# Optimization experiments

Hardware: AMD Instinct MI355X
Metric: run time of the kernel (lower is better)

## Reference

```python
import jax, jax.numpy as jnp
import numpy as np

N = 4096
D = 256
L = 4
B = 8


def _graph_norm(x, cums, gamma, beta_g, num_segments):
    # GraphNormGAT: per-graph mean / unbiased std over ragged segments.
    n = x.shape[0]
    seg = jnp.searchsorted(cums, jnp.arange(n), side='right') - 1  # [N] segment ids
    ones = jnp.ones((n,), x.dtype)
    cnt = jax.ops.segment_sum(ones, seg, num_segments=num_segments)[:, None]  # [B,1]
    mean = jax.ops.segment_sum(x, seg, num_segments=num_segments) / cnt       # [B,D]
    diff = x - mean[seg]
    var = jax.ops.segment_sum(diff * diff, seg, num_segments=num_segments) / jnp.maximum(cnt - 1.0, 1.0)
    std = jnp.sqrt(var)
    return gamma * (diff / (std[seg] + 1e-5)) + beta_g


def _mean_shift(beta, xyz, q, k, v, y_hat, mask, t, bw, use_std_att, self_distance, max_iter):
    # Distance-masked mean-shift attention: Gaussian kernel on coordinates
    # combined with QK attention; iteratively shifts xyz toward weighted mean.
    d = q.shape[-1]
    x_out = v
    for _ in range(max_iter):
        att = (q @ k.T) * (1.0 / (np.sqrt(d) * float(t)))  # [N,N]
        if use_std_att:
            m = att.mean(axis=-1, keepdims=True)
            s = att.std(axis=-1, keepdims=True)
            att = (att - m) / (s + 1e-5)
        sq = jnp.sum(xyz * xyz, axis=-1)
        d2 = jnp.maximum(sq[:, None] + sq[None, :] - 2.0 * (xyz @ xyz.T), 0.0)
        d2 = d2 + float(self_distance) * jnp.eye(xyz.shape[0], dtype=d2.dtype)
        logits = att - d2 / (2.0 * bw * bw) + jnp.log(y_hat.T + 1e-9)
        logits = jnp.where(mask, logits, -1e9)
        w = jax.nn.softmax(logits, axis=-1)  # [N,N]
        xyz = beta * (w @ xyz) + (1.0 - beta) * xyz
        x_out = w @ v
    return xyz, x_out


def setup_inputs() -> dict:
    key = jax.random.key(0)
    ks = jax.random.split(key, 12)
    inp = {}
    inp['xyz'] = jax.random.normal(ks[0], (N, 3), jnp.float32)
    inp['x'] = jax.random.normal(ks[1], (N, D), jnp.float32)
    inp['y_hat'] = jax.random.uniform(ks[2], (N, 1), jnp.float32)
    inp['distance_mask'] = jax.random.randint(ks[3], (N, N), 0, 2).astype(bool)
    inp['t'] = 1
    inp['band_width'] = jnp.ones((1,), jnp.float32)
    inp['beta'] = jax.random.uniform(ks[4], (1,), jnp.float32)
    inp['cums'] = jnp.arange(B + 1, dtype=jnp.int32) * (N // B)
    inp['big_inter_mask'] = jnp.ones((N, N), dtype=bool)
    inp['use_std_att'] = 1
    inp['self_distance'] = 10000
    scale = 1.0 / np.sqrt(D)
    inp['qw'] = jax.random.normal(ks[5], (L, D, D), jnp.float32) * scale
    inp['kw'] = jax.random.normal(ks[6], (L, D, D), jnp.float32) * scale
    inp['vw'] = jax.random.normal(ks[7], (L, D, D), jnp.float32) * scale
    inp['ow'] = jax.random.normal(ks[8], (L, D, D), jnp.float32) * scale
    inp['qb'] = jnp.zeros((L, D), jnp.float32)
    inp['kb'] = jnp.zeros((L, D), jnp.float32)
    inp['vb'] = jnp.zeros((L, D), jnp.float32)
    inp['ob'] = jnp.zeros((L, D), jnp.float32)
    inp['gamma'] = jnp.ones((L, 1, D), jnp.float32)
    inp['beta_g'] = jnp.zeros((L, 1, D), jnp.float32)
    return inp


def reference(xyz, x, y_hat, distance_mask, t, band_width, beta, cums,
              big_inter_mask, use_std_att, self_distance,
              qw, kw, vw, ow, qb, kb, vb, ob, gamma, beta_g):
    mask = distance_mask & big_inter_mask
    bw = band_width[0]
    bt = beta[0]
    for l in range(L):
        res = x
        q = x @ qw[l].T + qb[l]
        k = x @ kw[l].T + kb[l]
        v = x @ vw[l].T + vb[l]
        xyz, h = _mean_shift(bt, xyz, q, k, v, y_hat, mask, t, bw,
                             use_std_att, self_distance, max_iter=1)
        h = h @ ow[l].T + ob[l]
        x = res + h
        x = _graph_norm(x, cums, gamma[l], beta_g[l], num_segments=B)
    return x
```

## Files before the change

### kernel.cpp

```cpp
#include <hip/hip_runtime.h>
#include <hip/hip_bf16.h>
#include <math.h>

#define N_ROWS 4096
#define DIM    256
#define LDQ    288
#define NLAYER 4
#define GN_CHUNKS 16

typedef __attribute__((ext_vector_type(8))) short bf16x8;
typedef __attribute__((ext_vector_type(4))) float f32x4;
typedef unsigned short us;

__device__ __forceinline__ us f2b(float f) {
  unsigned int u = __float_as_uint(f);
  unsigned int r = (u + 0x7fffu + ((u >> 16) & 1u)) >> 16;
  return (us)r;
}
__device__ __forceinline__ float b2f(us b) {
  return __uint_as_float(((unsigned int)b) << 16);
}
__device__ __forceinline__ bf16x8 f8_to_b8(float4 a, float4 b) {
  bf16x8 r;
  r[0] = (short)f2b(a.x);
  r[1] = (short)f2b(a.y);
  r[2] = (short)f2b(a.z);
  r[3] = (short)f2b(a.w);
  r[4] = (short)f2b(b.x);
  r[5] = (short)f2b(b.y);
  r[6] = (short)f2b(b.z);
  r[7] = (short)f2b(b.w);
  return r;
}
__device__ __forceinline__ void gload16(const us* g, short* l) {
  __builtin_amdgcn_global_load_lds(
      (const __attribute__((address_space(1))) unsigned int*)g,
      (__attribute__((address_space(3))) unsigned int*)l, 16, 0, 0);
}

__global__ __launch_bounds__(256) void mfma_nt_kernel(
    const us* __restrict__ A, int lda, const us* __restrict__ Bb,
    const float* __restrict__ Bf, const float* __restrict__ bias,
    const float* __restrict__ res, float* __restrict__ C) {
  __shared__ __align__(16) short Al[64 * 32];
  __shared__ __align__(16) short Bl[64 * 32];
  const int tid = threadIdx.x;
  const int wv = tid >> 6, lane = tid & 63;
  const int cl = lane & 15, gq = lane >> 4;
  const int wr = wv >> 1, wc = wv & 1;
  const int m0 = blockIdx.x * 64, n0 = blockIdx.y * 64;
  f32x4 acc[2][2];
#pragma unroll
  for (int mi = 0; mi < 2; ++mi)
#pragma unroll
    for (int ni = 0; ni < 2; ++ni) acc[mi][ni] = (f32x4){0.f, 0.f, 0.f, 0.f};
  for (int k0 = 0; k0 < DIM; k0 += 32) {
    __syncthreads();
    {
      int r = tid >> 2, c = tid & 3;
      *(bf16x8*)&Al[r * 32 + c * 8] =
          *(const bf16x8*)&A[(size_t)(m0 + r) * lda + k0 + c * 8];
      if (Bf) {
        float4 u = *(const float4*)&Bf[(size_t)(n0 + r) * DIM + k0 + c * 8];
        float4 v =
            *(const float4*)&Bf[(size_t)(n0 + r) * DIM + k0 + c * 8 + 4];
        *(bf16x8*)&Bl[r * 32 + c * 8] = f8_to_b8(u, v);
      } else {
        *(bf16x8*)&Bl[r * 32 + c * 8] =
            *(const bf16x8*)&Bb[(size_t)(n0 + r) * DIM + k0 + c * 8];
      }
    }
    __syncthreads();
    bf16x8 af[2], bfr[2];
#pragma unroll
    for (int mi = 0; mi < 2; ++mi)
      af[mi] = *(const bf16x8*)&Al[(wr * 32 + mi * 16 + cl) * 32 + gq * 8];
#pragma unroll
    for (int ni = 0; ni < 2; ++ni)
      bfr[ni] = *(const bf16x8*)&Bl[(wc * 32 + ni * 16 + cl) * 32 + gq * 8];
#pragma unroll
    for (int mi = 0; mi < 2; ++mi)
#pragma unroll
      for (int ni = 0; ni < 2; ++ni)
        acc[mi][ni] = __builtin_amdgcn_mfma_f32_16x16x32_bf16(
            af[mi], bfr[ni], acc[mi][ni], 0, 0, 0);
  }
#pragma unroll
  for (int mi = 0; mi < 2; ++mi)
#pragma unroll
    for (int ni = 0; ni < 2; ++ni)
#pragma unroll
      for (int i = 0; i < 4; ++i) {
        int row = m0 + wr * 32 + mi * 16 + gq * 4 + i;
        int col = n0 + wc * 32 + ni * 16 + cl;
        float v = acc[mi][ni][i];
        if (bias) v += bias[col];
        if (res) v += res[(size_t)row * DIM + col];
        C[(size_t)row * DIM + col] = v;
      }
}

__global__ __launch_bounds__(256) void mfma_qkv_kernel(
    const float* __restrict__ A, const float* __restrict__ W0,
    const float* __restrict__ W1, const float* __restrict__ W2,
    const float* __restrict__ b0, const float* __restrict__ b1,
    const float* __restrict__ b2, us* __restrict__ O0, us* __restrict__ O1,
    us* __restrict__ O2) {
  const float* Bm = (blockIdx.z == 0) ? W0 : (blockIdx.z == 1) ? W1 : W2;
  const float* bias = (blockIdx.z == 0) ? b0 : (blockIdx.z == 1) ? b1 : b2;
  us* Ob = (blockIdx.z == 0) ? O0 : (blockIdx.z == 1) ? O1 : O2;
  const int ldo = (blockIdx.z == 2) ? DIM : LDQ;
  __shared__ __align__(16) short Al[64 * 32];
  __shared__ __align__(16) short Bl[64 * 32];
  const int tid = threadIdx.x;
  const int wv = tid >> 6, lane = tid & 63;
  const int cl = lane & 15, gq = lane >> 4;
  const int wr = wv >> 1, wc = wv & 1;
  const int m0 = blockIdx.x * 64, n0 = blockIdx.y * 64;
  f32x4 acc[2][2];
#pragma unroll
  for (int mi = 0; mi < 2; ++mi)
#pragma unroll
    for (int ni = 0; ni < 2; ++ni) acc[mi][ni] = (f32x4){0.f, 0.f, 0.f, 0.f};
  for (int k0 = 0; k0 < DIM; k0 += 32) {
    __syncthreads();
    {
      int r = tid >> 2, c = tid & 3;
      float4 ua = *(const float4*)&A[(size_t)(m0 + r) * DIM + k0 + c * 8];
      float4 va = *(const float4*)&A[(size_t)(m0 + r) * DIM + k0 + c * 8 + 4];
      *(bf16x8*)&Al[r * 32 + c * 8] = f8_to_b8(ua, va);
      float4 ub = *(const float4*)&Bm[(size_t)(n0 + r) * DIM + k0 + c * 8];
      float4 vb = *(const float4*)&Bm[(size_t)(n0 + r) * DIM + k0 + c * 8 + 4];
      *(bf16x8*)&Bl[r * 32 + c * 8] = f8_to_b8(ub, vb);
    }
    __syncthreads();
    bf16x8 af[2], bfr[2];
#pragma unroll
    for (int mi = 0; mi < 2; ++mi)
      af[mi] = *(const bf16x8*)&Al[(wr * 32 + mi * 16 + cl) * 32 + gq * 8];
#pragma unroll
    for (int ni = 0; ni < 2; ++ni)
      bfr[ni] = *(const bf16x8*)&Bl[(wc * 32 + ni * 16 + cl) * 32 + gq * 8];
#pragma unroll
    for (int mi = 0; mi < 2; ++mi)
#pragma unroll
      for (int ni = 0; ni < 2; ++ni)
        acc[mi][ni] = __builtin_amdgcn_mfma_f32_16x16x32_bf16(
            af[mi], bfr[ni], acc[mi][ni], 0, 0, 0);
  }
#pragma unroll
  for (int mi = 0; mi < 2; ++mi)
#pragma unroll
    for (int ni = 0; ni < 2; ++ni)
#pragma unroll
      for (int i = 0; i < 4; ++i) {
        int row = m0 + wr * 32 + mi * 16 + gq * 4 + i;
        int col = n0 + wc * 32 + ni * 16 + cl;
        Ob[(size_t)row * ldo + col] = f2b(acc[mi][ni][i] + bias[col]);
      }
}

__global__ __launch_bounds__(256) void mpart_mfma_kernel(
    const us* __restrict__ Kt, float* __restrict__ Mp) {
  __shared__ __align__(16) short Al[64 * 32];
  __shared__ __align__(16) short Bl[64 * 32];
  const int tid = threadIdx.x;
  const int wv = tid >> 6, lane = tid & 63;
  const int cl = lane & 15, gq = lane >> 4;
  const int wr = wv >> 1, wc = wv & 1;
  const int a0 = blockIdx.x * 64, b0 = blockIdx.y * 64;
  const int kb = blockIdx.z * 512;
  f32x4 acc[2][2];
#pragma unroll
  for (int mi = 0; mi < 2; ++mi)
#pragma unroll
    for (int ni = 0; ni < 2; ++ni) acc[mi][ni] = (f32x4){0.f, 0.f, 0.f, 0.f};
  for (int k0 = 0; k0 < 512; k0 += 32) {
    __syncthreads();
    {
      int r = tid >> 2, c = tid & 3;
      *(bf16x8*)&Al[r * 32 + c * 8] =
          *(const bf16x8*)&Kt[(size_t)(a0 + r) * N_ROWS + kb + k0 + c * 8];
      *(bf16x8*)&Bl[r * 32 + c * 8] =
          *(const bf16x8*)&Kt[(size_t)(b0 + r) * N_ROWS + kb + k0 + c * 8];
    }
    __syncthreads();
    bf16x8 af[2], bfr[2];
#pragma unroll
    for (int mi = 0; mi < 2; ++mi)
      af[mi] = *(const bf16x8*)&Al[(wr * 32 + mi * 16 + cl) * 32 + gq * 8];
#pragma unroll
    for (int ni = 0; ni < 2; ++ni)
      bfr[ni] = *(const bf16x8*)&Bl[(wc * 32 + ni * 16 + cl) * 32 + gq * 8];
#pragma unroll
    for (int mi = 0; mi < 2; ++mi)
#pragma unroll
      for (int ni = 0; ni < 2; ++ni)
        acc[mi][ni] = __builtin_amdgcn_mfma_f32_16x16x32_bf16(
            af[mi], bfr[ni], acc[mi][ni], 0, 0, 0);
  }
#pragma unroll
  for (int mi = 0; mi < 2; ++mi)
#pragma unroll
    for (int ni = 0; ni < 2; ++ni)
#pragma unroll
      for (int i = 0; i < 4; ++i) {
        int row = a0 + wr * 32 + mi * 16 + gq * 4 + i;
        int col = b0 + wc * 32 + ni * 16 + cl;
        Mp[(size_t)blockIdx.z * 65536 + (size_t)row * DIM + col] =
            acc[mi][ni][i];
      }
}

__global__ void mreduce_kernel(const float* __restrict__ Mp,
                               us* __restrict__ Mb) {
  int e = blockIdx.x * 256 + threadIdx.x;
  float s = 0.f;
#pragma unroll
  for (int z = 0; z < 8; ++z) s += Mp[(size_t)z * 65536 + e];
  Mb[e] = f2b(s);
}

__global__ void ksum_part_kernel(const us* __restrict__ K,
                                 float* __restrict__ kpart) {
  int d = threadIdx.x, b = blockIdx.x;
  float s = 0.f;
  int base = b * 64;
  for (int n = 0; n < 64; ++n) s += b2f(K[(size_t)(base + n) * LDQ + d]);
  kpart[b * DIM + d] = s;
}
__global__ void ksum_red_kernel(const float* __restrict__ kpart,
                                float* __restrict__ ksum) {
  int d = threadIdx.x;
  float s = 0.f;
  for (int b = 0; b < 64; ++b) s += kpart[b * DIM + d];
  ksum[d] = s;
}

__global__ __launch_bounds__(256) void stats_kernel(
    us* __restrict__ Qh, us* __restrict__ Kh, us* __restrict__ Vtb,
    const float* __restrict__ tb, const float* __restrict__ ksum,
    const float* __restrict__ xyzc, const float* __restrict__ logy,
    const int* __restrict__ tptr, const float* __restrict__ bwp,
    const int* __restrict__ usestdp, float* __restrict__ c1a,
    float* __restrict__ cAa, float* __restrict__ colB) {
  const int wave = threadIdx.x >> 6, lane = threadIdx.x & 63;
  const int row = blockIdx.x * 4 + wave;
  ushort4 q4 = *(const ushort4*)&Qh[(size_t)row * LDQ + lane * 4];
  float qx = b2f(q4.x), qy = b2f(q4.y), qz = b2f(q4.z), qw = b2f(q4.w);
  const float4 tv4 = ((const float4*)(tb + (size_t)row * DIM))[lane];
  const float4 kv = ((const float4*)ksum)[lane];
  float p1 = qx * kv.x + qy * kv.y + qz * kv.z + qw * kv.w;
  float p2 = tv4.x * qx + tv4.y * qy + tv4.z * qz + tv4.w * qw;
#pragma unroll
  for (int off = 32; off >= 1; off >>= 1) {
    p1 += __shfl_xor(p1, off);
    p2 += __shfl_xor(p2, off);
  }
  float tt = (float)tptr[0];
  float sc = 1.f / (16.f * tt);
  float mean = p1 * sc * (1.f / (float)N_ROWS);
  float e2 = p2 * sc * sc * (1.f / (float)N_ROWS);
  float var = fmaxf(e2 - mean * mean, 0.f);
  float istd = 1.f / (sqrtf(var) + 1e-5f);
  int usestd = usestdp[0];
  float c1 = usestd ? sc * istd : sc;
  float c2 = usestd ? -mean * istd : 0.f;
  float bw = bwp[0];
  float i2 = 1.f / (2.f * bw * bw);
  float t2 = 2.f * i2;
  float x0 = xyzc[(size_t)row * 3 + 0];
  float x1 = xyzc[(size_t)row * 3 + 1];
  float x2 = xyzc[(size_t)row * 3 + 2];
  float sq = x0 * x0 + x1 * x1 + x2 * x2;
  if (lane == 0) {
    c1a[row] = c1;
    cAa[row] = c2 - sq * i2;
    colB[row] = logy[row] - sq * i2;
  }
  float qs = t2 / c1;
  if (lane < 32) {
    float v = (lane == 0) ? qs * x0
              : (lane == 1) ? qs * x1
              : (lane == 2) ? qs * x2
                            : 0.f;
    Qh[(size_t)row * LDQ + 256 + lane] = (lane < 3) ? f2b(v) : 0;
  } else {
    int j = lane - 32;
    float v = (j == 0) ? x0 : (j == 1) ? x1 : (j == 2) ? x2 : 0.f;
    Kh[(size_t)row * LDQ + 256 + j] = (j < 3) ? f2b(v) : 0;
  }
  if (lane < 16) {
    us v = 0;
    if (lane == 0) v = f2b(x0);
    else if (lane == 1) v = f2b(x1);
    else if (lane == 2) v = f2b(x2);
    else if (lane == 3) v = 0x3F80;
    Vtb[(size_t)(256 + lane) * N_ROWS + row] = v;
  }
}

__global__ void prep_kernel(const float* __restrict__ yhat,
                            float* __restrict__ logy) {
  int i = blockIdx.x * 256 + threadIdx.x;
  logy[i] = logf(yhat[i] + 1e-9f);
}

__global__ void maskpack_kernel(const int* __restrict__ dmask,
                                const int* __restrict__ bmask,
                                unsigned int* __restrict__ mbits) {
  int gid = blockIdx.x * 256 + threadIdx.x;
  bool v = (dmask[gid] != 0) && (bmask[gid] != 0);
  unsigned long long bal = __ballot(v);
  if ((threadIdx.x & 63) == 0) {
    int w = gid >> 5;
    mbits[w] = (unsigned int)(bal & 0xffffffffu);
    mbits[w + 1] = (unsigned int)(bal >> 32);
  }
}

__global__ __launch_bounds__(256) void vt2_kernel(const us* __restrict__ inK,
                                                  const us* __restrict__ inV,
                                                  us* __restrict__ outK,
                                                  us* __restrict__ outV) {
  __shared__ us T[64][68];
  const us* in = (blockIdx.z == 0) ? inK : inV;
  us* out = (blockIdx.z == 0) ? outK : outV;
  const int lda = (blockIdx.z == 0) ? LDQ : DIM;
  const int n0 = blockIdx.x * 64, d0 = blockIdx.y * 64;
  const int tx = threadIdx.x & 63, ty = threadIdx.x >> 6;
#pragma unroll
  for (int p = 0; p < 16; ++p)
    T[ty + p * 4][tx] = in[(size_t)(n0 + ty + p * 4) * lda + d0 + tx];
  __syncthreads();
#pragma unroll
  for (int p = 0; p < 16; ++p)
    out[(size_t)(d0 + ty + p * 4) * N_ROWS + n0 + tx] = T[tx][ty + p * 4];
}

__global__ __launch_bounds__(256, 2) void flash5_kernel(
    const us* __restrict__ Qh, const us* __restrict__ Kh,
    const us* __restrict__ Vtb, const float* __restrict__ colB,
    const float* __restrict__ c1a, const float* __restrict__ cAa,
    const unsigned int* __restrict__ mbits, const float* __restrict__ bwp,
    const int* __restrict__ selfdp, us* __restrict__ plo, us* __restrict__ phi,
    float* __restrict__ ps, float* __restrict__ paxlo,
    float* __restrict__ paxhi, int cps) {
  __shared__ __align__(16) short SMEM[22528];
  short* Pl = SMEM + 18432;

  const int tid = threadIdx.x;
  const int wv = tid >> 6, lane = tid & 63;
  const int cl = lane & 15, gq = lane >> 4;
  const int split = blockIdx.x;
  const int R0 = blockIdx.y * 64 + wv * 16;
  const int colbase = split * cps;

  const float bw = bwp[0];
  const float i2 = 1.f / (2.f * bw * bw);
  const float sd2 = (float)selfdp[0] * i2;

  bf16x8 qa[9];
  {
    const bf16x8* qp = (const bf16x8*)(Qh + (size_t)(R0 + cl) * LDQ);
#pragma unroll
    for (int ks = 0; ks < 9; ++ks) qa[ks] = qp[ks * 4 + gq];
  }
  float c1v[4], cAv[4];
#pragma unroll
  for (int i = 0; i < 4; ++i) {
    int row = R0 + gq * 4 + i;
    c1v[i] = c1a[row];
    cAv[i] = cAa[row];
  }
  f32x4 o[17];
#pragma unroll
  for (int dt = 0; dt < 17; ++dt) o[dt] = (f32x4){0.f, 0.f, 0.f, 0.f};

  auto stage = [&](int t0g, int b) {
    short* base = SMEM + b * 9216;
#pragma unroll
    for (int p = 0; p < 5; ++p) {
      int L = tid + p * 256;
      if (L < 1152) {
        int ks = L >> 7, ct = (L >> 6) & 1, g = (L >> 4) & 3, c = L & 15;
        gload16(&Kh[(size_t)(t0g + 2 * c + ct) * LDQ + ks * 32 + g * 8],
                &base[L * 8]);
      }
    }
  };

  stage(colbase, 0);
  __syncthreads();
  int cur = 0;

  for (int tt = 0; tt < cps; tt += 32) {
    const int t0g = colbase + tt;
    if (tt + 32 < cps) stage(t0g + 32, cur ^ 1);
    const short* Khl = SMEM + cur * 9216;

    const int gc0 = t0g + 2 * cl;
    const float cb0 = colB[gc0];
    const float cb1 = colB[gc0 + 1];

    f32x4 s0 = (f32x4){0.f, 0.f, 0.f, 0.f};
    f32x4 s1 = (f32x4){0.f, 0.f, 0.f, 0.f};
#pragma unroll
    for (int ks = 0; ks < 9; ++ks) {
      bf16x8 kf = *(const bf16x8*)&Khl[(ks * 128 + gq * 16 + cl) * 8];
      s0 = __builtin_amdgcn_mfma_f32_16x16x32_bf16(qa[ks], kf, s0, 0, 0, 0);
    }
#pragma unroll
    for (int ks = 0; ks < 9; ++ks) {
      bf16x8 kf = *(const bf16x8*)&Khl[(ks * 128 + 64 + gq * 16 + cl) * 8];
      s1 = __builtin_amdgcn_mfma_f32_16x16x32_bf16(qa[ks], kf, s1, 0, 0, 0);
    }

#pragma unroll
    for (int i = 0; i < 4; ++i) {
      int row = R0 + gq * 4 + i;
      unsigned int mw = mbits[((size_t)row << 7) + (t0g >> 5)];
      unsigned int pm = (mw >> (2 * cl)) & 3u;
      float lg0 = fmaf(s0[i], c1v[i], cAv[i] + cb0);
      float lg1 = fmaf(s1[i], c1v[i], cAv[i] + cb1);
      if (row == gc0) lg0 -= sd2;
      if (row == gc0 + 1) lg1 -= sd2;
      lg0 = (pm & 1u) ? lg0 : -60.f;
      lg1 = (pm & 2u) ? lg1 : -60.f;
      float p0 = __expf(lg0);
      float p1 = __expf(lg1);
      unsigned int pk = (unsigned int)f2b(p0) | ((unsigned int)f2b(p1) << 16);
      *(unsigned int*)&Pl[wv * 512 + ((cl >> 2) * 16 + gq * 4 + i) * 8 +
                          (cl & 3) * 2] = pk;
    }
    bf16x8 pf = *(const bf16x8*)&Pl[wv * 512 + (gq * 16 + cl) * 8];
#pragma unroll
    for (int dt = 0; dt < 17; ++dt) {
      bf16x8 vf =
          *(const bf16x8*)&Vtb[(size_t)(dt * 16 + cl) * N_ROWS + t0g + gq * 8];
      o[dt] = __builtin_amdgcn_mfma_f32_16x16x32_bf16(pf, vf, o[dt], 0, 0, 0);
    }
    __syncthreads();
    cur ^= 1;
  }

  us* pb = (split < 8) ? plo : phi;
  float* paxb = (split < 8) ? paxlo : paxhi;
  const int sl = split & 7;
  short* obuf = SMEM + wv * 4096;
#pragma unroll
  for (int dt = 0; dt < 16; ++dt)
#pragma unroll
    for (int i = 0; i < 4; ++i)
      obuf[(gq * 4 + i) * 256 + dt * 16 + cl] = (short)f2b(o[dt][i]);
#pragma unroll
  for (int p = 0; p < 8; ++p) {
    int idx = p * 512 + lane * 8;
    int rl = idx >> 8;
    int col = idx & 255;
    bf16x8 v = *(const bf16x8*)&obuf[idx];
    *(bf16x8*)&pb[((size_t)sl * N_ROWS + R0 + rl) * DIM + col] = v;
  }
#pragma unroll
  for (int i = 0; i < 4; ++i) {
    int row = R0 + gq * 4 + i;
    float aug = o[16][i];
    if (cl < 3)
      paxb[((size_t)sl * N_ROWS + row) * 3 + cl] = aug;
    else if (cl == 3)
      ps[(size_t)split * N_ROWS + row] = aug;
  }
}

__global__ __launch_bounds__(256) void merge_kernel(
    const us* __restrict__ plo, const us* __restrict__ phi,
    const float* __restrict__ ps, const float* __restrict__ paxlo,
    const float* __restrict__ paxhi, const float* __restrict__ xyzc,
    const float* __restrict__ betap, us* __restrict__ xattb,
    float* __restrict__ xyz_out, int nsplit) {
  const int wvl = threadIdx.x >> 6, lane = threadIdx.x & 63;
  const int row = blockIdx.x * 4 + wvl;
  float den = 0.f;
  for (int k = 0; k < nsplit; ++k) den += ps[(size_t)k * N_ROWS + row];
  float inv = 1.f / den;
  float a0 = 0.f, a1 = 0.f, a2 = 0.f, a3 = 0.f;
  float axs = 0.f;
  for (int k = 0; k < nsplit; ++k) {
    const us* pb = (k < 8) ? plo : phi;
    const us* p = &pb[((size_t)(k & 7) * N_ROWS + row) * DIM + lane * 4];
    uint2 u = *(const uint2*)p;
    a0 += __uint_as_float((u.x & 0xffffu) << 16);
    a1 += __uint_as_float(u.x & 0xffff0000u);
    a2 += __uint_as_float((u.y & 0xffffu) << 16);
    a3 += __uint_as_float(u.y & 0xffff0000u);
    if (lane < 3) {
      const float* paxb = (k < 8) ? paxlo : paxhi;
      axs += paxb[((size_t)(k & 7) * N_ROWS + row) * 3 + lane];
    }
  }
  ushort4 ov;
  ov.x = f2b(a0 * inv);
  ov.y = f2b(a1 * inv);
  ov.z = f2b(a2 * inv);
  ov.w = f2b(a3 * inv);
  *(ushort4*)&xattb[(size_t)row * DIM + lane * 4] = ov;
  if (lane < 3) {
    float beta = betap[0];
    xyz_out[(size_t)row * 3 + lane] =
        beta * axs * inv + (1.f - beta) * xyzc[(size_t)row * 3 + lane];
  }
}

__global__ __launch_bounds__(256) void gn_part_kernel(
    const float* __restrict__ X, const int* __restrict__ cums,
    float* __restrict__ gpart) {
  const int seg = blockIdx.x, chunk = blockIdx.y, d = threadIdx.x;
  const int r0 = cums[seg], r1 = cums[seg + 1];
  const int cnt = r1 - r0;
  const int per = (cnt + GN_CHUNKS - 1) / GN_CHUNKS;
  const int a = r0 + chunk * per;
  const int b = min(a + per, r1);
  float s = 0.f, ss = 0.f;
  for (int r = a; r < b; ++r) {
    float v = X[(size_t)r * DIM + d];
    s += v;
    ss += v * v;
  }
  gpart[(((size_t)seg * GN_CHUNKS + chunk) * 2 + 0) * DIM + d] = s;
  gpart[(((size_t)seg * GN_CHUNKS + chunk) * 2 + 1) * DIM + d] = ss;
}

__global__ void gn_red_kernel(const float* __restrict__ gpart,
                              const int* __restrict__ cums,
                              float* __restrict__ gm, float* __restrict__ gi) {
  const int seg = blockIdx.x, d = threadIdx.x;
  float s = 0.f, ss = 0.f;
#pragma unroll
  for (int c = 0; c < GN_CHUNKS; ++c) {
    s += gpart[(((size_t)seg * GN_CHUNKS + c) * 2 + 0) * DIM + d];
    ss += gpart[(((size_t)seg * GN_CHUNKS + c) * 2 + 1) * DIM + d];
  }
  float cnt = (float)(cums[seg + 1] - cums[seg]);
  float mean = s / fmaxf(cnt, 1.f);
  float var = (ss - cnt * mean * mean) / fmaxf(cnt - 1.f, 1.f);
  gm[seg * DIM + d] = mean;
  gi[seg * DIM + d] = 1.f / (sqrtf(fmaxf(var, 0.f)) + 1e-5f);
}

__global__ __launch_bounds__(256) void gn_apply_kernel(
    const float* __restrict__ X, const float* __restrict__ gamma,
    const float* __restrict__ betag, const int* __restrict__ cums, int nseg,
    const float* __restrict__ gm, const float* __restrict__ gi,
    float* __restrict__ Xout, float* __restrict__ ofinal) {
  int idx = blockIdx.x * 256 + threadIdx.x;
  int base = idx * 4;
  int row = base >> 8, d0 = base & 255;
  int seg = 0;
  for (int b = 1; b <= nseg; ++b) seg += (row >= cums[b]) ? 1 : 0;
  float4 x = ((const float4*)X)[idx];
  float xs[4] = {x.x, x.y, x.z, x.w};
  const float* gmp = gm + seg * DIM + d0;
  const float* gip = gi + seg * DIM + d0;
  float o[4];
#pragma unroll
  for (int c = 0; c < 4; ++c)
    o[c] = gamma[d0 + c] * (xs[c] - gmp[c]) * gip[c] + betag[d0 + c];
  float4 ov = {o[0], o[1], o[2], o[3]};
  ((float4*)Xout)[idx] = ov;
  if (ofinal) ((float4*)ofinal)[idx] = ov;
}

extern "C" void kernel_launch(void* const* d_in, const int* in_sizes, int n_in,
                              void* d_out, int out_size, void* d_ws,
                              size_t ws_size, hipStream_t stream) {
  const float* xyz0 = (const float*)d_in[0];
  const float* x0 = (const float*)d_in[1];
  const float* yhat = (const float*)d_in[2];
  const int* dmask = (const int*)d_in[3];
  const int* tptr = (const int*)d_in[4];
  const float* bwp = (const float*)d_in[5];
  const float* betap = (const float*)d_in[6];
  const int* cums = (const int*)d_in[7];
  const int* bmask = (const int*)d_in[8];
  const int* usestdp = (const int*)d_in[9];
  const int* selfdp = (const int*)d_in[10];
  const float* qw = (const float*)d_in[11];
  const float* kw = (const float*)d_in[12];
  const float* vw = (const float*)d_in[13];
  const float* ow = (const float*)d_in[14];
  const float* qbv = (const float*)d_in[15];
  const float* kbv = (const float*)d_in[16];
  const float* vbv = (const float*)d_in[17];
  const float* obv = (const float*)d_in[18];
  const float* gamma = (const float*)d_in[19];
  const float* betag = (const float*)d_in[20];
  float* out = (float*)d_out;
  float* ws = (float*)d_ws;

  const size_t ND = (size_t)N_ROWS * DIM;

  us* Vb16 = (us*)ws;
  float* bt = ws;
  us* plo = (us*)ws;
  us* Qh = (us*)(ws + 4 * ND);
  us* Kh = Qh + (size_t)N_ROWS * LDQ;
  us* Vtb = Kh + (size_t)N_ROWS * LDQ;
  unsigned int* mbits = (unsigned int*)(Vtb + (size_t)272 * N_ROWS);
  float* kpart = (float*)(mbits + (size_t)N_ROWS * 128);
  float* ksum = kpart + 64 * DIM;
  float* c1a = ksum + DIM;
  float* cAa = c1a + N_ROWS;
  float* colB = cAa + N_ROWS;
  float* logy = colB + N_ROWS;
  float* xyzA = logy + N_ROWS;
  float* xyzB = xyzA + 3 * N_ROWS;
  float* gm = xyzB + 3 * N_ROWS;
  float* gi = gm + 8 * DIM;
  float* gpart = gi + 8 * DIM;
  float* psbase = gpart + 8 * GN_CHUNKS * 2 * DIM;
  float* paxlo = psbase + 16 * (size_t)N_ROWS;
  float* paxhi = paxlo + 8 * (size_t)N_ROWS * 3;
  us* Mb16 = (us*)(paxhi + 8 * (size_t)N_ROWS * 3);
  float* Pend = (float*)(Mb16 + 65536);
  float* bo = Pend;
  us* Ktb = (us*)(bo + ND);
  float* Mp = (float*)(Ktb + (size_t)256 * N_ROWS);
  us* phi = (us*)Pend;
  us* xattb = Ktb;
  const size_t P0w = (size_t)(Pend - ws);
  const size_t full16 = (P0w + 5 * ND) * 4;
  const int nsplit = (ws_size >= full16) ? 16 : 8;
  const int cps = N_ROWS / nsplit;
  float* bx = Pend + (size_t)(nsplit == 16 ? 4 : 2) * ND;

  const int nseg = in_sizes[7] - 1;

  prep_kernel<<<16, 256, 0, stream>>>(yhat, logy);
  maskpack_kernel<<<65536, 256, 0, stream>>>(dmask, bmask, mbits);

  for (int l = 0; l < NLAYER; ++l) {
    const float* xin = (l == 0) ? x0 : bx;
    const float* xyz_in = (l == 0) ? xyz0 : ((l & 1) ? xyzB : xyzA);
    float* xyz_o = (l & 1) ? xyzA : xyzB;
    const size_t wo = (size_t)l * DIM * DIM;

    mfma_qkv_kernel<<<dim3(64, 4, 3), 256, 0, stream>>>(
        xin, qw + wo, kw + wo, vw + wo, qbv + l * DIM, kbv + l * DIM,
        vbv + l * DIM, Qh, Kh, Vb16);
    ksum_part_kernel<<<64, 256, 0, stream>>>(Kh, kpart);
    vt2_kernel<<<dim3(64, 4, 2), 256, 0, stream>>>(Kh, Vb16, Ktb, Vtb);
    ksum_red_kernel<<<1, 256, 0, stream>>>(kpart, ksum);
    mpart_mfma_kernel<<<dim3(4, 4, 8), 256, 0, stream>>>(Ktb, Mp);
    mreduce_kernel<<<256, 256, 0, stream>>>(Mp, Mb16);
    mfma_nt_kernel<<<dim3(64, 4), 256, 0, stream>>>(Qh, LDQ, Mb16, nullptr,
                                                    nullptr, nullptr, bt);
    stats_kernel<<<1024, 256, 0, stream>>>(Qh, Kh, Vtb, bt, ksum, xyz_in, logy,
                                           tptr, bwp, usestdp, c1a, cAa, colB);
    flash5_kernel<<<dim3(nsplit, 64), 256, 0, stream>>>(
        Qh, Kh, Vtb, colB, c1a, cAa, mbits, bwp, selfdp, plo, phi, psbase,
        paxlo, paxhi, cps);
    merge_kernel<<<1024, 256, 0, stream>>>(plo, phi, psbase, paxlo, paxhi,
                                           xyz_in, betap, xattb, xyz_o,
                                           nsplit);
    mfma_nt_kernel<<<dim3(64, 4), 256, 0, stream>>>(
        xattb, DIM, nullptr, ow + wo, obv + l * DIM, xin, bo);
    gn_part_kernel<<<dim3(nseg, GN_CHUNKS), 256, 0, stream>>>(bo, cums, gpart);
    gn_red_kernel<<<nseg, 256, 0, stream>>>(gpart, cums, gm, gi);
    gn_apply_kernel<<<1024, 256, 0, stream>>>(
        bo, gamma + (size_t)l * DIM, betag + (size_t)l * DIM, cums, nseg, gm,
        gi, bx, (l == NLAYER - 1) ? out : nullptr);
  }
}
```

Before: 738.9 us.

## Stage 64 key columns per flash iteration, single-pass ksum, deeper split-K for M

The flash attention kernel now stages two 32-column key tiles per double-buffered step, roughly doubling shared memory, so it needs half as many barriers and loop iterations. The two-kernel K column-sum is replaced by one kernel that reduces each row of the transposed K with wave shuffles. The K^T K partial product is split across 32 slices instead of 8 when 16 flash splits are used, to expose more blocks. The costs are higher LDS use, which may limit occupancy, and a larger Mp scratch buffer that must fit in the workspace.

```diff
diff --git a/kernel.cpp b/kernel.cpp
--- a/kernel.cpp
+++ b/kernel.cpp
@@ -161,7 +161,7 @@
 }
 
 __global__ __launch_bounds__(256) void mpart_mfma_kernel(
-    const us* __restrict__ Kt, float* __restrict__ Mp) {
+    const us* __restrict__ Kt, float* __restrict__ Mp, int cpz) {
   __shared__ __align__(16) short Al[64 * 32];
   __shared__ __align__(16) short Bl[64 * 32];
   const int tid = threadIdx.x;
@@ -169,13 +169,13 @@
   const int cl = lane & 15, gq = lane >> 4;
   const int wr = wv >> 1, wc = wv & 1;
   const int a0 = blockIdx.x * 64, b0 = blockIdx.y * 64;
-  const int kb = blockIdx.z * 512;
+  const int kb = blockIdx.z * cpz;
   f32x4 acc[2][2];
 #pragma unroll
   for (int mi = 0; mi < 2; ++mi)
 #pragma unroll
     for (int ni = 0; ni < 2; ++ni) acc[mi][ni] = (f32x4){0.f, 0.f, 0.f, 0.f};
-  for (int k0 = 0; k0 < 512; k0 += 32) {
+  for (int k0 = 0; k0 < cpz; k0 += 32) {
     __syncthreads();
     {
       int r = tid >> 2, c = tid & 3;
@@ -213,28 +213,25 @@
 }
 
 __global__ void mreduce_kernel(const float* __restrict__ Mp,
-                               us* __restrict__ Mb) {
+                               us* __restrict__ Mb, int mz) {
   int e = blockIdx.x * 256 + threadIdx.x;
   float s = 0.f;
-#pragma unroll
-  for (int z = 0; z < 8; ++z) s += Mp[(size_t)z * 65536 + e];
+  for (int z = 0; z < mz; ++z) s += Mp[(size_t)z * 65536 + e];
   Mb[e] = f2b(s);
 }
 
-__global__ void ksum_part_kernel(const us* __restrict__ K,
-                                 float* __restrict__ kpart) {
-  int d = threadIdx.x, b = blockIdx.x;
+__global__ __launch_bounds__(256) void ksum2_kernel(const us* __restrict__ Ktb,
+                                                    float* __restrict__ ksum) {
+  __shared__ float red[4];
+  const int d = blockIdx.x;
+  const us* row = Ktb + (size_t)d * N_ROWS;
   float s = 0.f;
-  int base = b * 64;
-  for (int n = 0; n < 64; ++n) s += b2f(K[(size_t)(base + n) * LDQ + d]);
-  kpart[b * DIM + d] = s;
-}
-__global__ void ksum_red_kernel(const float* __restrict__ kpart,
-                                float* __restrict__ ksum) {
-  int d = threadIdx.x;
-  float s = 0.f;
-  for (int b = 0; b < 64; ++b) s += kpart[b * DIM + d];
-  ksum[d] = s;
+  for (int i = threadIdx.x; i < N_ROWS; i += 256) s += b2f(row[i]);
+#pragma unroll
+  for (int off = 32; off >= 1; off >>= 1) s += __shfl_xor(s, off);
+  if ((threadIdx.x & 63) == 0) red[threadIdx.x >> 6] = s;
+  __syncthreads();
+  if (threadIdx.x == 0) ksum[d] = (red[0] + red[1]) + (red[2] + red[3]);
 }
 
 __global__ __launch_bounds__(256) void stats_kernel(
@@ -346,8 +343,8 @@
     const int* __restrict__ selfdp, us* __restrict__ plo, us* __restrict__ phi,
     float* __restrict__ ps, float* __restrict__ paxlo,
     float* __restrict__ paxhi, int cps) {
-  __shared__ __align__(16) short SMEM[22528];
-  short* Pl = SMEM + 18432;
+  __shared__ __align__(16) short SMEM[38912];
+  short* Pl = SMEM + 36864;
 
   const int tid = threadIdx.x;
   const int wv = tid >> 6, lane = tid & 63;
@@ -378,15 +375,16 @@
   for (int dt = 0; dt < 17; ++dt) o[dt] = (f32x4){0.f, 0.f, 0.f, 0.f};
 
   auto stage = [&](int t0g, int b) {
-    short* base = SMEM + b * 9216;
-#pragma unroll
-    for (int p = 0; p < 5; ++p) {
+    short* base = SMEM + b * 18432;
+#pragma unroll
+    for (int p = 0; p < 9; ++p) {
       int L = tid + p * 256;
-      if (L < 1152) {
-        int ks = L >> 7, ct = (L >> 6) & 1, g = (L >> 4) & 3, c = L & 15;
-        gload16(&Kh[(size_t)(t0g + 2 * c + ct) * LDQ + ks * 32 + g * 8],
-                &base[L * 8]);
-      }
+      int sub = (L >= 1152) ? 1 : 0;
+      int L2 = L - sub * 1152;
+      int ks = L2 >> 7, ct = (L2 >> 6) & 1, g = (L2 >> 4) & 3, c = L2 & 15;
+      gload16(
+          &Kh[(size_t)(t0g + sub * 32 + 2 * c + ct) * LDQ + ks * 32 + g * 8],
+          &base[L * 8]);
     }
   };
 
@@ -394,51 +392,59 @@
   __syncthreads();
   int cur = 0;
 
-  for (int tt = 0; tt < cps; tt += 32) {
+  for (int tt = 0; tt < cps; tt += 64) {
     const int t0g = colbase + tt;
-    if (tt + 32 < cps) stage(t0g + 32, cur ^ 1);
-    const short* Khl = SMEM + cur * 9216;
-
-    const int gc0 = t0g + 2 * cl;
-    const float cb0 = colB[gc0];
-    const float cb1 = colB[gc0 + 1];
-
-    f32x4 s0 = (f32x4){0.f, 0.f, 0.f, 0.f};
-    f32x4 s1 = (f32x4){0.f, 0.f, 0.f, 0.f};
-#pragma unroll
-    for (int ks = 0; ks < 9; ++ks) {
-      bf16x8 kf = *(const bf16x8*)&Khl[(ks * 128 + gq * 16 + cl) * 8];
-      s0 = __builtin_amdgcn_mfma_f32_16x16x32_bf16(qa[ks], kf, s0, 0, 0, 0);
-    }
-#pragma unroll
-    for (int ks = 0; ks < 9; ++ks) {
-      bf16x8 kf = *(const bf16x8*)&Khl[(ks * 128 + 64 + gq * 16 + cl) * 8];
-      s1 = __builtin_amdgcn_mfma_f32_16x16x32_bf16(qa[ks], kf, s1, 0, 0, 0);
-    }
-
-#pragma unroll
-    for (int i = 0; i < 4; ++i) {
-      int row = R0 + gq * 4 + i;
-      unsigned int mw = mbits[((size_t)row << 7) + (t0g >> 5)];
-      unsigned int pm = (mw >> (2 * cl)) & 3u;
-      float lg0 = fmaf(s0[i], c1v[i], cAv[i] + cb0);
-      float lg1 = fmaf(s1[i], c1v[i], cAv[i] + cb1);
-      if (row == gc0) lg0 -= sd2;
-      if (row == gc0 + 1) lg1 -= sd2;
-      lg0 = (pm & 1u) ? lg0 : -60.f;
-      lg1 = (pm & 2u) ? lg1 : -60.f;
-      float p0 = __expf(lg0);
-      float p1 = __expf(lg1);
-      unsigned int pk = (unsigned int)f2b(p0) | ((unsigned int)f2b(p1) << 16);
-      *(unsigned int*)&Pl[wv * 512 + ((cl >> 2) * 16 + gq * 4 + i) * 8 +
-                          (cl & 3) * 2] = pk;
-    }
-    bf16x8 pf = *(const bf16x8*)&Pl[wv * 512 + (gq * 16 + cl) * 8];
-#pragma unroll
-    for (int dt = 0; dt < 17; ++dt) {
-      bf16x8 vf =
-          *(const bf16x8*)&Vtb[(size_t)(dt * 16 + cl) * N_ROWS + t0g + gq * 8];
-      o[dt] = __builtin_amdgcn_mfma_f32_16x16x32_bf16(pf, vf, o[dt], 0, 0, 0);
+    if (tt + 64 < cps) stage(t0g + 64, cur ^ 1);
+    const short* Kb0 = SMEM + cur * 18432;
+
+#pragma unroll
+    for (int sub = 0; sub < 2; ++sub) {
+      const short* Khl = Kb0 + sub * 9216;
+      const int tg = t0g + sub * 32;
+      const int gc0 = tg + 2 * cl;
+      const float cb0 = colB[gc0];
+      const float cb1 = colB[gc0 + 1];
+
+      f32x4 s0 = (f32x4){0.f, 0.f, 0.f, 0.f};
+      f32x4 s1 = (f32x4){0.f, 0.f, 0.f, 0.f};
+#pragma unroll
+      for (int ks = 0; ks < 9; ++ks) {
+        bf16x8 kf = *(const bf16x8*)&Khl[(ks * 128 + gq * 16 + cl) * 8];
+        s0 = __builtin_amdgcn_mfma_f32_16x16x32_bf16(qa[ks], kf, s0, 0, 0, 0);
+      }
+#pragma unroll
+      for (int ks = 0; ks < 9; ++ks) {
+        bf16x8 kf = *(const bf16x8*)&Khl[(ks * 128 + 64 + gq * 16 + cl) * 8];
+        s1 = __builtin_amdgcn_mfma_f32_16x16x32_bf16(qa[ks], kf, s1, 0, 0, 0);
+      }
+
+#pragma unroll
+      for (int i = 0; i < 4; ++i) {
+        int row = R0 + gq * 4 + i;
+        unsigned int mw = mbits[((size_t)row << 7) + (tg >> 5)];
+        unsigned int pm = (mw >> (2 * cl)) & 3u;
+        float lg0 = fmaf(s0[i], c1v[i], cAv[i] + cb0);
+        float lg1 = fmaf(s1[i], c1v[i], cAv[i] + cb1);
+        if (row == gc0) lg0 -= sd2;
+        if (row == gc0 + 1) lg1 -= sd2;
+        lg0 = (pm & 1u) ? lg0 : -60.f;
+        lg1 = (pm & 2u) ? lg1 : -60.f;
+        float p0 = __expf(lg0);
+        float p1 = __expf(lg1);
+        unsigned int pk =
+            (unsigned int)f2b(p0) | ((unsigned int)f2b(p1) << 16);
+        *(unsigned int*)&Pl[wv * 512 + ((cl >> 2) * 16 + gq * 4 + i) * 8 +
+                            (cl & 3) * 2] = pk;
+      }
+      bf16x8 pf = *(const bf16x8*)&Pl[wv * 512 + (gq * 16 + cl) * 8];
+#pragma unroll
+      for (int dt = 0; dt < 17; ++dt) {
+        bf16x8 vf =
+            *(const bf16x8*)&Vtb[(size_t)(dt * 16 + cl) * N_ROWS + tg +
+                                 gq * 8];
+        o[dt] = __builtin_amdgcn_mfma_f32_16x16x32_bf16(pf, vf, o[dt], 0, 0,
+                                                        0);
+      }
     }
     __syncthreads();
     cur ^= 1;
@@ -631,6 +637,8 @@
   const size_t full16 = (P0w + 5 * ND) * 4;
   const int nsplit = (ws_size >= full16) ? 16 : 8;
   const int cps = N_ROWS / nsplit;
+  const int mz = (nsplit == 16) ? 32 : 8;
+  const int cpz = N_ROWS / mz;
   float* bx = Pend + (size_t)(nsplit == 16 ? 4 : 2) * ND;
 
   const int nseg = in_sizes[7] - 1;
@@ -647,11 +655,10 @@
     mfma_qkv_kernel<<<dim3(64, 4, 3), 256, 0, stream>>>(
         xin, qw + wo, kw + wo, vw + wo, qbv + l * DIM, kbv + l * DIM,
         vbv + l * DIM, Qh, Kh, Vb16);
-    ksum_part_kernel<<<64, 256, 0, stream>>>(Kh, kpart);
     vt2_kernel<<<dim3(64, 4, 2), 256, 0, stream>>>(Kh, Vb16, Ktb, Vtb);
-    ksum_red_kernel<<<1, 256, 0, stream>>>(kpart, ksum);
-    mpart_mfma_kernel<<<dim3(4, 4, 8), 256, 0, stream>>>(Ktb, Mp);
-    mreduce_kernel<<<256, 256, 0, stream>>>(Mp, Mb16);
+    ksum2_kernel<<<256, 256, 0, stream>>>(Ktb, ksum);
+    mpart_mfma_kernel<<<dim3(4, 4, mz), 256, 0, stream>>>(Ktb, Mp, cpz);
+    mreduce_kernel<<<256, 256, 0, stream>>>(Mp, Mb16, mz);
     mfma_nt_kernel<<<dim3(64, 4), 256, 0, stream>>>(Qh, LDQ, Mb16, nullptr,
                                                     nullptr, nullptr, bt);
     stats_kernel<<<1024, 256, 0, stream>>>(Qh, Kh, Vtb, bt, ksum, xyz_in, logy,
```

New measurement: 769.0 us. 1.04x slower.
